# Kernel tuning notes

Measured on AMD Instinct MI355X. Metric: run time of the kernel, lower is better.

## Reference

```python
import jax, jax.numpy as jnp
import numpy as np

B, C, DM, H = 2, 256, 512, 8
D = DM // H          # d_head = 64
SPARSE_K = 64


def setup_inputs() -> dict:
    key = jax.random.key(0)
    ks = jax.random.split(key, 12)
    s = 0.02
    return {
        "x": jax.random.normal(ks[0], (B, C, DM), dtype=jnp.float32),
        "Wq": jax.random.normal(ks[1], (DM, DM), dtype=jnp.float32) * s,
        "bq": jnp.zeros((DM,), jnp.float32),
        "Wk": jax.random.normal(ks[2], (DM, DM), dtype=jnp.float32) * s,
        "bk": jnp.zeros((DM,), jnp.float32),
        "Wv": jax.random.normal(ks[3], (DM, DM), dtype=jnp.float32) * s,
        "bv": jnp.zeros((DM,), jnp.float32),
        "w1": jax.random.normal(ks[4], (D, 3 * D), dtype=jnp.float32) * s,
        "b1": jax.random.normal(ks[5], (D,), dtype=jnp.float32) * s,
        "w2": jax.random.normal(ks[6], (1, D), dtype=jnp.float32) * s,
        "b2": jax.random.normal(ks[7], (1,), dtype=jnp.float32) * s,
        "Wo": jax.random.normal(ks[8], (DM, DM), dtype=jnp.float32) * s,
        "bo": jnp.zeros((DM,), jnp.float32),
    }


def _heads(x, W, b):
    # torch Linear: x @ W.T + b, then (B,C,H,d) -> (B,H,C,d)
    y = jnp.einsum("bcD,ED->bcE", x, W) + b
    return y.reshape(B, C, H, D).transpose(0, 2, 1, 3)


def reference(x, Wq, bq, Wk, bk, Wv, bv, w1, b1, w2, b2, Wo, bo):
    q = _heads(x, Wq, bq)  # (B,H,C,d)
    k = _heads(x, Wk, bk)
    v = _heads(x, Wv, bv)

    # split first MLP layer weight: [:, :d] acts on q, [:, d:2d] on k, [:, 2d:] on q*k
    q_p = jnp.einsum("bhcd,ed->bhce", q, w1[:, :D])
    k_p = jnp.einsum("bhcd,ed->bhce", k, w1[:, D:2 * D])

    # res: (B,H,C,C,d)
    res = q_p[:, :, :, None, :] + k_p[:, :, None, :, :] + b1
    interaction = q[:, :, :, None, :] * k[:, :, None, :, :]
    res = res + jnp.einsum("bhije,fe->bhijf", interaction, w1[:, 2 * D:])

    # second MLP layer -> scalar score per pair, exact (erf) GELU as torch default
    h = jax.nn.gelu(res, approximate=False)
    scores = (jnp.einsum("bhijd,od->bhijo", h, w2) + b2)[..., 0]
    scores = scores / jnp.sqrt(jnp.float32(D))

    if SPARSE_K < C:
        top_vals = jax.lax.top_k(scores, SPARSE_K)[0]
        thresh = top_vals[..., -1:]
        scores = jnp.where(scores >= thresh, scores, jnp.float32(-1e9))

    attn = jax.nn.softmax(scores, axis=-1)  # dropout is identity (p=0 / eval)
    out = jnp.einsum("bhij,bhjd->bhid", attn, v)
    out = out.transpose(0, 2, 1, 3).reshape(B, C, DM)
    return jnp.einsum("bcD,ED->bcE", out, Wo) + bo
```

## Files before the change

### kernel.cpp

```cpp
#include <hip/hip_runtime.h>
#include <math.h>

typedef _Float16 fp16;
typedef __attribute__((ext_vector_type(4))) _Float16 f16x4;
typedef __attribute__((ext_vector_type(8))) _Float16 f16x8;
typedef __attribute__((ext_vector_type(4))) float floatx4;
typedef __attribute__((ext_vector_type(2))) float f32x2;

__device__ __forceinline__ f32x2 mk2(float a, float b) { f32x2 r; r.x = a; r.y = b; return r; }
__device__ __forceinline__ f32x2 sp2(float a) { f32x2 r; r.x = a; r.y = a; return r; }

__device__ __forceinline__ f32x2 gelu2(f32x2 x) {
    f32x2 tt = x * 0.70710678118654752440f;
    f32x2 s  = tt * tt;
    f32x2 p  = __builtin_elementwise_fma(s, sp2(-8.548327023450852e-4f), sp2(5.223977625442188e-3f));
    p = __builtin_elementwise_fma(s, p, sp2(-2.6866170645131252e-2f));
    p = __builtin_elementwise_fma(s, p, sp2(0.11283791670955126f));
    p = __builtin_elementwise_fma(s, p, sp2(-0.3761263890318375f));
    p = __builtin_elementwise_fma(s, p, sp2(1.1283791670955126f));
    f32x2 e = tt * p;
    if (__builtin_expect(fabsf(tt.x) > 0.5f, 0)) e.x = erff(tt.x);
    if (__builtin_expect(fabsf(tt.y) > 0.5f, 0)) e.y = erff(tt.y);
    f32x2 hx = x * 0.5f;
    return __builtin_elementwise_fma(hx, e, hx);
}

__device__ __forceinline__ void split2(float a, fp16& h, fp16& m) {
    h = (fp16)a;
    m = (fp16)(a - (float)h);
}

struct SplitArgs {
    const float* src[5];
    fp16* h[5]; fp16* m[5];
};

__global__ __launch_bounds__(256) void split2_512_kernel(SplitArgs S) {
    int z = blockIdx.z;
    const float* src = S.src[z];
    fp16* dh = S.h[z]; fp16* dm = S.m[z];
    int t = blockIdx.x * 256 + threadIdx.x;
    int row = t >> 7, kq = (t & 127) * 4;
    int rt = row >> 4, rm = row & 15;
    int ks = kq >> 5, q4 = (kq >> 3) & 3, u0 = kq & 7;
    int dst = ((rt * 16 + ks) * 64 + q4 * 16 + rm) * 8 + u0;
    float4 vv = *(const float4*)&src[row * 512 + kq];
    float a4[4] = {vv.x, vv.y, vv.z, vv.w};
    f16x4 h, m;
    #pragma unroll
    for (int u = 0; u < 4; u++) {
        fp16 hh, mm;
        split2(a4[u], hh, mm);
        h[u] = hh; m[u] = mm;
    }
    *(f16x4*)&dh[dst] = h;
    *(f16x4*)&dm[dst] = m;
}

struct MM2Args {
    const fp16 *Ah, *Am;
    const fp16 *Wh[3], *Wm[3];
    const float* bias[3];
    float* outf[3];
    fp16 *kh, *km;
    int mode[3];
};

__global__ __launch_bounds__(64) void mm_mfma_kernel(MM2Args A) {
    const int z = blockIdx.z;
    const fp16* Wh = A.Wh[z]; const fp16* Wm = A.Wm[z];
    const float* bias = A.bias[z];
    const int lane = threadIdx.x;
    const int m16 = lane & 15, q4 = lane >> 4;
    const int mt = blockIdx.y, bx = blockIdx.x;

    floatx4 acc0, acc1;
    {
        float bv = bias[bx * 16 + m16];
        acc0[0] = bv; acc0[1] = bv; acc0[2] = bv; acc0[3] = bv;
        acc1[0] = 0.f; acc1[1] = 0.f; acc1[2] = 0.f; acc1[3] = 0.f;
    }

    #pragma unroll 4
    for (int ks = 0; ks < 16; ks++) {
        int sa = ((mt * 16 + ks) * 64 + lane) * 8;
        f16x8 ah = *(const f16x8*)&A.Ah[sa];
        f16x8 am = *(const f16x8*)&A.Am[sa];
        int sw = ((bx * 16 + ks) * 64 + lane) * 8;
        f16x8 wh = *(const f16x8*)&Wh[sw];
        f16x8 wm = *(const f16x8*)&Wm[sw];
        acc0 = __builtin_amdgcn_mfma_f32_16x16x32_f16(ah, wh, acc0, 0, 0, 0);
        acc1 = __builtin_amdgcn_mfma_f32_16x16x32_f16(ah, wm, acc1, 0, 0, 0);
        acc0 = __builtin_amdgcn_mfma_f32_16x16x32_f16(am, wh, acc0, 0, 0, 0);
        acc1 = __builtin_amdgcn_mfma_f32_16x16x32_f16(am, wm, acc1, 0, 0, 0);
    }
    floatx4 acc = acc0 + acc1;

    const int mode = A.mode[z];
    const int n = bx * 16 + m16;
    #pragma unroll
    for (int r = 0; r < 4; r++) {
        int m = mt * 16 + q4 * 4 + r;
        float val = acc[r];
        if (mode == 0) {
            A.outf[z][m * 512 + n] = val;
        } else if (mode == 1) {
            A.outf[z][(((m >> 8) * 8 + (n >> 6)) * 256 + (m & 255)) * 64 + (n & 63)] = val;
        } else {
            int krow = ((m >> 8) * 8 + (n >> 6)) * 256 + (m & 255);
            int d = n & 63;
            int dst = (((krow >> 4) * 2 + (d >> 5)) * 64 + ((d >> 3) & 3) * 16 + (krow & 15)) * 8 + (d & 7);
            fp16 h, mm;
            split2(val, h, mm);
            A.kh[dst] = h; A.km[dst] = mm;
        }
    }
}

__global__ __launch_bounds__(256, 4) void fused_mfma_attn_kernel(
    const float* __restrict__ q, const float* __restrict__ v,
    const fp16* __restrict__ khi, const fp16* __restrict__ kmid,
    const float* __restrict__ w1, const float* __restrict__ b1,
    const float* __restrict__ w2, const float* __restrict__ b2,
    fp16* __restrict__ oh, fp16* __restrict__ om)
{
    const int i2 = blockIdx.x;
    const int bh = blockIdx.y;
    const int t  = threadIdx.x;
    const int lane = t & 63, w = t >> 6;
    const int m16 = lane & 15, q4 = lane >> 4;

    __shared__ f32x2 part2[4][256];
    __shared__ f32x2 sc2[256];
    __shared__ float qpb_s[2][64];
    __shared__ f32x2 sbuf2[256];
    __shared__ f32x2 red_s[4][64];
    __shared__ f32x2 red2_s[4];
    __shared__ f32x2 thr_s2, smax_s2;

    const int f = w * 16 + m16;
    const float* w1row = w1 + f * 192;

    f16x8 Ah[2][2], Am[2][2];
    #pragma unroll
    for (int i01 = 0; i01 < 2; i01++) {
        const float* qrow = q + (bh * 256 + i2 * 2 + i01) * 64;
        float qa = 0.f;
        #pragma unroll
        for (int ks = 0; ks < 2; ks++) {
            int e0 = ks * 32 + q4 * 8;
            #pragma unroll
            for (int u = 0; u < 2; u++) {
                int e = e0 + u * 4;
                float4 wa = *(const float4*)&w1row[e];
                float4 wb = *(const float4*)&w1row[64 + e];
                float4 wc = *(const float4*)&w1row[128 + e];
                float4 qv = *(const float4*)&qrow[e];
                qa += wa.x * qv.x + wa.y * qv.y + wa.z * qv.z + wa.w * qv.w;
                float av[4];
                av[0] = fmaf(wc.x, qv.x, wb.x);
                av[1] = fmaf(wc.y, qv.y, wb.y);
                av[2] = fmaf(wc.z, qv.z, wb.z);
                av[3] = fmaf(wc.w, qv.w, wb.w);
                #pragma unroll
                for (int uu = 0; uu < 4; uu++) {
                    fp16 h, m;
                    split2(av[uu], h, m);
                    Ah[i01][ks][u * 4 + uu] = h;
                    Am[i01][ks][u * 4 + uu] = m;
                }
            }
        }
        qa += __shfl_xor(qa, 16);
        qa += __shfl_xor(qa, 32);
        if (lane < 16) qpb_s[i01][w * 16 + lane] = qa + b1[w * 16 + lane];
    }
    __syncthreads();

    floatx4 qpbr[2];
    qpbr[0] = *(const floatx4*)&qpb_s[0][w * 16 + q4 * 4];
    qpbr[1] = *(const floatx4*)&qpb_s[1][w * 16 + q4 * 4];
    const float4 w2f = *(const float4*)&w2[w * 16 + q4 * 4];
    const float b2v = b2[0];

    {
        int base = ((bh * 16) * 2 * 64 + lane) * 8;
        f16x8 Kh0 = *(const f16x8*)&khi [base];
        f16x8 Km0 = *(const f16x8*)&kmid[base];
        f16x8 Kh1 = *(const f16x8*)&khi [base + 512];
        f16x8 Km1 = *(const f16x8*)&kmid[base + 512];
        #pragma unroll 1
        for (int jt = 0; jt < 16; jt++) {
            f16x8 nKh0, nKm0, nKh1, nKm1;
            if (jt < 15) {
                int nb = ((bh * 16 + jt + 1) * 2 * 64 + lane) * 8;
                nKh0 = *(const f16x8*)&khi [nb];
                nKm0 = *(const f16x8*)&kmid[nb];
                nKh1 = *(const f16x8*)&khi [nb + 512];
                nKm1 = *(const f16x8*)&kmid[nb + 512];
            }
            floatx4 a0 = qpbr[0], a1 = qpbr[1];
            floatx4 b0, b1v_;
            b0[0] = 0.f; b0[1] = 0.f; b0[2] = 0.f; b0[3] = 0.f;
            b1v_ = b0;
            a0   = __builtin_amdgcn_mfma_f32_16x16x32_f16(Ah[0][0], Kh0, a0,   0, 0, 0);
            a1   = __builtin_amdgcn_mfma_f32_16x16x32_f16(Ah[1][0], Kh0, a1,   0, 0, 0);
            b0   = __builtin_amdgcn_mfma_f32_16x16x32_f16(Ah[0][0], Km0, b0,   0, 0, 0);
            b1v_ = __builtin_amdgcn_mfma_f32_16x16x32_f16(Ah[1][0], Km0, b1v_, 0, 0, 0);
            a0   = __builtin_amdgcn_mfma_f32_16x16x32_f16(Am[0][0], Kh0, a0,   0, 0, 0);
            a1   = __builtin_amdgcn_mfma_f32_16x16x32_f16(Am[1][0], Kh0, a1,   0, 0, 0);
            b0   = __builtin_amdgcn_mfma_f32_16x16x32_f16(Am[0][0], Km0, b0,   0, 0, 0);
            b1v_ = __builtin_amdgcn_mfma_f32_16x16x32_f16(Am[1][0], Km0, b1v_, 0, 0, 0);
            a0   = __builtin_amdgcn_mfma_f32_16x16x32_f16(Ah[0][1], Kh1, a0,   0, 0, 0);
            a1   = __builtin_amdgcn_mfma_f32_16x16x32_f16(Ah[1][1], Kh1, a1,   0, 0, 0);
            b0   = __builtin_amdgcn_mfma_f32_16x16x32_f16(Ah[0][1], Km1, b0,   0, 0, 0);
            b1v_ = __builtin_amdgcn_mfma_f32_16x16x32_f16(Ah[1][1], Km1, b1v_, 0, 0, 0);
            a0   = __builtin_amdgcn_mfma_f32_16x16x32_f16(Am[0][1], Kh1, a0,   0, 0, 0);
            a1   = __builtin_amdgcn_mfma_f32_16x16x32_f16(Am[1][1], Kh1, a1,   0, 0, 0);
            b0   = __builtin_amdgcn_mfma_f32_16x16x32_f16(Am[0][1], Km1, b0,   0, 0, 0);
            b1v_ = __builtin_amdgcn_mfma_f32_16x16x32_f16(Am[1][1], Km1, b1v_, 0, 0, 0);
            a0 = a0 + b0; a1 = a1 + b1v_;
            f32x2 g0 = gelu2(mk2(a0[0], a1[0]));
            f32x2 g1 = gelu2(mk2(a0[1], a1[1]));
            f32x2 g2 = gelu2(mk2(a0[2], a1[2]));
            f32x2 g3 = gelu2(mk2(a0[3], a1[3]));
            f32x2 sA = __builtin_elementwise_fma(g1, sp2(w2f.y), g0 * w2f.x);
            f32x2 sB = __builtin_elementwise_fma(g3, sp2(w2f.w), g2 * w2f.z);
            f32x2 s = sA + sB;
            s.x += __shfl_xor(s.x, 16);
            s.y += __shfl_xor(s.y, 16);
            s.x += __shfl_xor(s.x, 32);
            s.y += __shfl_xor(s.y, 32);
            if (lane < 16) part2[w][jt * 16 + lane] = s;
            Kh0 = nKh0; Km0 = nKm0; Kh1 = nKh1; Km1 = nKm1;
        }
    }
    __syncthreads();

    f32x2 score = ((part2[0][t] + part2[1][t]) + (part2[2][t] + part2[3][t]) + b2v) * 0.125f;

    f32x2 sv = score;
    #pragma unroll
    for (int k = 2; k <= 256; k <<= 1) {
        #pragma unroll
        for (int j = k >> 1; j >= 1; j >>= 1) {
            f32x2 pv;
            if (j >= 64) {
                sbuf2[t] = sv;
                __syncthreads();
                pv = sbuf2[t ^ j];
                __syncthreads();
            } else {
                pv.x = __shfl_xor(sv.x, j);
                pv.y = __shfl_xor(sv.y, j);
            }
            bool keepMin = (((t & j) == 0) == ((t & k) == 0));
            f32x2 mn = __builtin_elementwise_min(sv, pv);
            f32x2 mx = __builtin_elementwise_max(sv, pv);
            sv = keepMin ? mn : mx;
        }
    }
    if (t == 192) thr_s2  = sv;
    if (t == 255) smax_s2 = sv;
    __syncthreads();

    float p0 = (score.x >= thr_s2.x) ? __expf(score.x - smax_s2.x) : 0.0f;
    float p1 = (score.y >= thr_s2.y) ? __expf(score.y - smax_s2.y) : 0.0f;
    sc2[t] = mk2(p0, p1);
    f32x2 ps = mk2(p0, p1);
    #pragma unroll
    for (int mask = 1; mask < 64; mask <<= 1) {
        ps.x += __shfl_xor(ps.x, mask);
        ps.y += __shfl_xor(ps.y, mask);
    }
    if (lane == 0) red2_s[w] = ps;
    __syncthreads();
    f32x2 den = (red2_s[0] + red2_s[1]) + (red2_s[2] + red2_s[3]);
    f32x2 invp = mk2(1.0f / den.x, 1.0f / den.y);

    const int d = t & 63, g = t >> 6;
    const float* vb = v + bh * 256 * 64;
    f32x2 av = mk2(0.f, 0.f), avb = mk2(0.f, 0.f);
    for (int j8 = 0; j8 < 8; j8++) {
        int jj = g * 64 + j8 * 8;
        f32x2 pp0 = sc2[jj + 0];
        f32x2 pp1 = sc2[jj + 1];
        f32x2 pp2 = sc2[jj + 2];
        f32x2 pp3 = sc2[jj + 3];
        f32x2 pp4 = sc2[jj + 4];
        f32x2 pp5 = sc2[jj + 5];
        f32x2 pp6 = sc2[jj + 6];
        f32x2 pp7 = sc2[jj + 7];
        float v0 = vb[(jj + 0) * 64 + d];
        float v1 = vb[(jj + 1) * 64 + d];
        float v2 = vb[(jj + 2) * 64 + d];
        float v3 = vb[(jj + 3) * 64 + d];
        float v4 = vb[(jj + 4) * 64 + d];
        float v5 = vb[(jj + 5) * 64 + d];
        float v6 = vb[(jj + 6) * 64 + d];
        float v7 = vb[(jj + 7) * 64 + d];
        av  = __builtin_elementwise_fma(pp0, sp2(v0), av);
        avb = __builtin_elementwise_fma(pp4, sp2(v4), avb);
        av  = __builtin_elementwise_fma(pp1, sp2(v1), av);
        avb = __builtin_elementwise_fma(pp5, sp2(v5), avb);
        av  = __builtin_elementwise_fma(pp2, sp2(v2), av);
        avb = __builtin_elementwise_fma(pp6, sp2(v6), avb);
        av  = __builtin_elementwise_fma(pp3, sp2(v3), av);
        avb = __builtin_elementwise_fma(pp7, sp2(v7), avb);
    }
    red_s[g][d] = av + avb;
    __syncthreads();

    if (t < 128) {
        int i01 = t >> 6, dd = t & 63;
        f32x2 osum = (red_s[0][dd] + red_s[1][dd]) + (red_s[2][dd] + red_s[3][dd]);
        float o = (i01 ? osum.y : osum.x) * (i01 ? invp.y : invp.x);
        int b = bh >> 3, h = bh & 7;
        int row = b * 256 + i2 * 2 + i01;
        int n = h * 64 + dd;
        int dst = (((row >> 4) * 16 + (n >> 5)) * 64 + ((n >> 3) & 3) * 16 + (row & 15)) * 8 + (n & 7);
        fp16 hh, mm;
        split2(o, hh, mm);
        oh[dst] = hh; om[dst] = mm;
    }
}

extern "C" void kernel_launch(void* const* d_in, const int* in_sizes, int n_in,
                              void* d_out, int out_size, void* d_ws, size_t ws_size,
                              hipStream_t stream) {
    const float* x  = (const float*)d_in[0];
    const float* Wq = (const float*)d_in[1];
    const float* bq = (const float*)d_in[2];
    const float* Wk = (const float*)d_in[3];
    const float* bk = (const float*)d_in[4];
    const float* Wv = (const float*)d_in[5];
    const float* bv = (const float*)d_in[6];
    const float* w1 = (const float*)d_in[7];
    const float* b1 = (const float*)d_in[8];
    const float* w2 = (const float*)d_in[9];
    const float* b2 = (const float*)d_in[10];
    const float* Wo = (const float*)d_in[11];
    const float* bo = (const float*)d_in[12];
    float* out = (float*)d_out;

    const int NE = 262144;
    float* qb  = (float*)d_ws;
    float* vb  = qb + NE;
    fp16* base = (fp16*)(vb + NE);
    fp16* khi  = base;            fp16* kmid = khi + NE;
    fp16* xs   = kmid + NE;
    fp16* wqs  = xs  + 2 * NE;
    fp16* wks  = wqs + 2 * NE;
    fp16* wvs  = wks + 2 * NE;
    fp16* wos  = wvs + 2 * NE;
    fp16* oas  = wos + 2 * NE;

    {
        SplitArgs S;
        const float* srcs[5] = {x, Wq, Wk, Wv, Wo};
        fp16* dsts[5] = {xs, wqs, wks, wvs, wos};
        for (int z = 0; z < 5; z++) {
            S.src[z] = srcs[z];
            S.h[z] = dsts[z]; S.m[z] = dsts[z] + NE;
        }
        split2_512_kernel<<<dim3(256, 1, 5), 256, 0, stream>>>(S);
    }
    {
        MM2Args M;
        M.Ah = xs; M.Am = xs + NE;
        M.Wh[0] = wqs; M.Wm[0] = wqs + NE;
        M.Wh[1] = wks; M.Wm[1] = wks + NE;
        M.Wh[2] = wvs; M.Wm[2] = wvs + NE;
        M.bias[0] = bq; M.bias[1] = bk; M.bias[2] = bv;
        M.outf[0] = qb; M.outf[1] = nullptr; M.outf[2] = vb;
        M.kh = khi; M.km = kmid;
        M.mode[0] = 1; M.mode[1] = 2; M.mode[2] = 1;
        mm_mfma_kernel<<<dim3(32, 32, 3), 64, 0, stream>>>(M);
    }
    fused_mfma_attn_kernel<<<dim3(128, 16), 256, 0, stream>>>(
        qb, vb, khi, kmid, w1, b1, w2, b2,
        oas, oas + NE);
    {
        MM2Args M;
        M.Ah = oas; M.Am = oas + NE;
        M.Wh[0] = wos; M.Wm[0] = wos + NE;
        M.Wh[1] = wos; M.Wm[1] = wos;
        M.Wh[2] = wos; M.Wm[2] = wos;
        M.bias[0] = bo; M.bias[1] = bo; M.bias[2] = bo;
        M.outf[0] = out; M.outf[1] = out; M.outf[2] = out;
        M.kh = khi; M.km = kmid;
        M.mode[0] = 0; M.mode[1] = 0; M.mode[2] = 0;
        mm_mfma_kernel<<<dim3(32, 32, 1), 64, 0, stream>>>(M);
    }
}
```

Baseline: 173.2 us.

## Process four query rows per attention block to reuse K fragments

```diff
diff --git a/kernel.cpp b/kernel.cpp
--- a/kernel.cpp
+++ b/kernel.cpp
@@ -117,46 +117,45 @@
     }
 }
 
-__global__ __launch_bounds__(256, 4) void fused_mfma_attn_kernel(
+__global__ __launch_bounds__(256, 3) void fused_mfma_attn_kernel(
     const float* __restrict__ q, const float* __restrict__ v,
     const fp16* __restrict__ khi, const fp16* __restrict__ kmid,
     const float* __restrict__ w1, const float* __restrict__ b1,
     const float* __restrict__ w2, const float* __restrict__ b2,
     fp16* __restrict__ oh, fp16* __restrict__ om)
 {
-    const int i2 = blockIdx.x;
+    const int i4 = blockIdx.x;
     const int bh = blockIdx.y;
     const int t  = threadIdx.x;
     const int lane = t & 63, w = t >> 6;
     const int m16 = lane & 15, q4 = lane >> 4;
 
-    __shared__ f32x2 part2[4][256];
-    __shared__ f32x2 sc2[256];
-    __shared__ float qpb_s[2][64];
-    __shared__ f32x2 sbuf2[256];
-    __shared__ f32x2 red_s[4][64];
-    __shared__ f32x2 red2_s[4];
-    __shared__ f32x2 thr_s2, smax_s2;
+    __shared__ f32x2 part2[2][4][256];
+    __shared__ f32x2 sc2[2][256];
+    __shared__ float qpb_s[4][64];
+    __shared__ f32x2 sbuf2[2][256];
+    __shared__ f32x2 red_s[2][4][64];
+    __shared__ f32x2 red2_s[2][4];
+    __shared__ f32x2 thr_s2[2], smax_s2[2];
 
     const int f = w * 16 + m16;
     const float* w1row = w1 + f * 192;
 
-    f16x8 Ah[2][2], Am[2][2];
-    #pragma unroll
-    for (int i01 = 0; i01 < 2; i01++) {
-        const float* qrow = q + (bh * 256 + i2 * 2 + i01) * 64;
-        float qa = 0.f;
+    f16x8 Ah[4][2], Am[4][2];
+    float qa[4] = {0.f, 0.f, 0.f, 0.f};
+    const float* qbase = q + (bh * 256 + i4 * 4) * 64;
+    #pragma unroll
+    for (int ks = 0; ks < 2; ks++) {
         #pragma unroll
-        for (int ks = 0; ks < 2; ks++) {
-            int e0 = ks * 32 + q4 * 8;
+        for (int u = 0; u < 2; u++) {
+            int e = ks * 32 + q4 * 8 + u * 4;
+            float4 wa = *(const float4*)&w1row[e];
+            float4 wb = *(const float4*)&w1row[64 + e];
+            float4 wc = *(const float4*)&w1row[128 + e];
             #pragma unroll
-            for (int u = 0; u < 2; u++) {
-                int e = e0 + u * 4;
-                float4 wa = *(const float4*)&w1row[e];
-                float4 wb = *(const float4*)&w1row[64 + e];
-                float4 wc = *(const float4*)&w1row[128 + e];
-                float4 qv = *(const float4*)&qrow[e];
-                qa += wa.x * qv.x + wa.y * qv.y + wa.z * qv.z + wa.w * qv.w;
+            for (int i01 = 0; i01 < 4; i01++) {
+                float4 qv = *(const float4*)&qbase[i01 * 64 + e];
+                qa[i01] += wa.x * qv.x + wa.y * qv.y + wa.z * qv.z + wa.w * qv.w;
                 float av[4];
                 av[0] = fmaf(wc.x, qv.x, wb.x);
                 av[1] = fmaf(wc.y, qv.y, wb.y);
@@ -171,15 +170,20 @@
                 }
             }
         }
-        qa += __shfl_xor(qa, 16);
-        qa += __shfl_xor(qa, 32);
-        if (lane < 16) qpb_s[i01][w * 16 + lane] = qa + b1[w * 16 + lane];
+    }
+    #pragma unroll
+    for (int i01 = 0; i01 < 4; i01++) {
+        float qaa = qa[i01];
+        qaa += __shfl_xor(qaa, 16);
+        qaa += __shfl_xor(qaa, 32);
+        if (lane < 16) qpb_s[i01][w * 16 + lane] = qaa + b1[w * 16 + lane];
     }
     __syncthreads();
 
-    floatx4 qpbr[2];
-    qpbr[0] = *(const floatx4*)&qpb_s[0][w * 16 + q4 * 4];
-    qpbr[1] = *(const floatx4*)&qpb_s[1][w * 16 + q4 * 4];
+    floatx4 qpbr[4];
+    #pragma unroll
+    for (int i01 = 0; i01 < 4; i01++)
+        qpbr[i01] = *(const floatx4*)&qpb_s[i01][w * 16 + q4 * 4];
     const float4 w2f = *(const float4*)&w2[w * 16 + q4 * 4];
     const float b2v = b2[0];
 
@@ -199,98 +203,110 @@
                 nKh1 = *(const f16x8*)&khi [nb + 512];
                 nKm1 = *(const f16x8*)&kmid[nb + 512];
             }
-            floatx4 a0 = qpbr[0], a1 = qpbr[1];
-            floatx4 b0, b1v_;
-            b0[0] = 0.f; b0[1] = 0.f; b0[2] = 0.f; b0[3] = 0.f;
-            b1v_ = b0;
-            a0   = __builtin_amdgcn_mfma_f32_16x16x32_f16(Ah[0][0], Kh0, a0,   0, 0, 0);
-            a1   = __builtin_amdgcn_mfma_f32_16x16x32_f16(Ah[1][0], Kh0, a1,   0, 0, 0);
-            b0   = __builtin_amdgcn_mfma_f32_16x16x32_f16(Ah[0][0], Km0, b0,   0, 0, 0);
-            b1v_ = __builtin_amdgcn_mfma_f32_16x16x32_f16(Ah[1][0], Km0, b1v_, 0, 0, 0);
-            a0   = __builtin_amdgcn_mfma_f32_16x16x32_f16(Am[0][0], Kh0, a0,   0, 0, 0);
-            a1   = __builtin_amdgcn_mfma_f32_16x16x32_f16(Am[1][0], Kh0, a1,   0, 0, 0);
-            b0   = __builtin_amdgcn_mfma_f32_16x16x32_f16(Am[0][0], Km0, b0,   0, 0, 0);
-            b1v_ = __builtin_amdgcn_mfma_f32_16x16x32_f16(Am[1][0], Km0, b1v_, 0, 0, 0);
-            a0   = __builtin_amdgcn_mfma_f32_16x16x32_f16(Ah[0][1], Kh1, a0,   0, 0, 0);
-            a1   = __builtin_amdgcn_mfma_f32_16x16x32_f16(Ah[1][1], Kh1, a1,   0, 0, 0);
-            b0   = __builtin_amdgcn_mfma_f32_16x16x32_f16(Ah[0][1], Km1, b0,   0, 0, 0);
-            b1v_ = __builtin_amdgcn_mfma_f32_16x16x32_f16(Ah[1][1], Km1, b1v_, 0, 0, 0);
-            a0   = __builtin_amdgcn_mfma_f32_16x16x32_f16(Am[0][1], Kh1, a0,   0, 0, 0);
-            a1   = __builtin_amdgcn_mfma_f32_16x16x32_f16(Am[1][1], Kh1, a1,   0, 0, 0);
-            b0   = __builtin_amdgcn_mfma_f32_16x16x32_f16(Am[0][1], Km1, b0,   0, 0, 0);
-            b1v_ = __builtin_amdgcn_mfma_f32_16x16x32_f16(Am[1][1], Km1, b1v_, 0, 0, 0);
-            a0 = a0 + b0; a1 = a1 + b1v_;
-            f32x2 g0 = gelu2(mk2(a0[0], a1[0]));
-            f32x2 g1 = gelu2(mk2(a0[1], a1[1]));
-            f32x2 g2 = gelu2(mk2(a0[2], a1[2]));
-            f32x2 g3 = gelu2(mk2(a0[3], a1[3]));
-            f32x2 sA = __builtin_elementwise_fma(g1, sp2(w2f.y), g0 * w2f.x);
-            f32x2 sB = __builtin_elementwise_fma(g3, sp2(w2f.w), g2 * w2f.z);
-            f32x2 s = sA + sB;
-            s.x += __shfl_xor(s.x, 16);
-            s.y += __shfl_xor(s.y, 16);
-            s.x += __shfl_xor(s.x, 32);
-            s.y += __shfl_xor(s.y, 32);
-            if (lane < 16) part2[w][jt * 16 + lane] = s;
+            #pragma unroll
+            for (int p = 0; p < 2; p++) {
+                const int ia = 2 * p, ib = 2 * p + 1;
+                floatx4 a0 = qpbr[ia], a1 = qpbr[ib];
+                floatx4 b0, b1v_;
+                b0[0] = 0.f; b0[1] = 0.f; b0[2] = 0.f; b0[3] = 0.f;
+                b1v_ = b0;
+                a0   = __builtin_amdgcn_mfma_f32_16x16x32_f16(Ah[ia][0], Kh0, a0,   0, 0, 0);
+                a1   = __builtin_amdgcn_mfma_f32_16x16x32_f16(Ah[ib][0], Kh0, a1,   0, 0, 0);
+                b0   = __builtin_amdgcn_mfma_f32_16x16x32_f16(Ah[ia][0], Km0, b0,   0, 0, 0);
+                b1v_ = __builtin_amdgcn_mfma_f32_16x16x32_f16(Ah[ib][0], Km0, b1v_, 0, 0, 0);
+                a0   = __builtin_amdgcn_mfma_f32_16x16x32_f16(Am[ia][0], Kh0, a0,   0, 0, 0);
+                a1   = __builtin_amdgcn_mfma_f32_16x16x32_f16(Am[ib][0], Kh0, a1,   0, 0, 0);
+                b0   = __builtin_amdgcn_mfma_f32_16x16x32_f16(Am[ia][0], Km0, b0,   0, 0, 0);
+                b1v_ = __builtin_amdgcn_mfma_f32_16x16x32_f16(Am[ib][0], Km0, b1v_, 0, 0, 0);
+                a0   = __builtin_amdgcn_mfma_f32_16x16x32_f16(Ah[ia][1], Kh1, a0,   0, 0, 0);
+                a1   = __builtin_amdgcn_mfma_f32_16x16x32_f16(Ah[ib][1], Kh1, a1,   0, 0, 0);
+                b0   = __builtin_amdgcn_mfma_f32_16x16x32_f16(Ah[ia][1], Km1, b0,   0, 0, 0);
+                b1v_ = __builtin_amdgcn_mfma_f32_16x16x32_f16(Ah[ib][1], Km1, b1v_, 0, 0, 0);
+                a0   = __builtin_amdgcn_mfma_f32_16x16x32_f16(Am[ia][1], Kh1, a0,   0, 0, 0);
+                a1   = __builtin_amdgcn_mfma_f32_16x16x32_f16(Am[ib][1], Kh1, a1,   0, 0, 0);
+                b0   = __builtin_amdgcn_mfma_f32_16x16x32_f16(Am[ia][1], Km1, b0,   0, 0, 0);
+                b1v_ = __builtin_amdgcn_mfma_f32_16x16x32_f16(Am[ib][1], Km1, b1v_, 0, 0, 0);
+                a0 = a0 + b0; a1 = a1 + b1v_;
+                f32x2 g0 = gelu2(mk2(a0[0], a1[0]));
+                f32x2 g1 = gelu2(mk2(a0[1], a1[1]));
+                f32x2 g2 = gelu2(mk2(a0[2], a1[2]));
+                f32x2 g3 = gelu2(mk2(a0[3], a1[3]));
+                f32x2 sA = __builtin_elementwise_fma(g1, sp2(w2f.y), g0 * w2f.x);
+                f32x2 sB = __builtin_elementwise_fma(g3, sp2(w2f.w), g2 * w2f.z);
+                f32x2 s = sA + sB;
+                s.x += __shfl_xor(s.x, 16);
+                s.y += __shfl_xor(s.y, 16);
+                s.x += __shfl_xor(s.x, 32);
+                s.y += __shfl_xor(s.y, 32);
+                if (lane < 16) part2[p][w][jt * 16 + lane] = s;
+            }
             Kh0 = nKh0; Km0 = nKm0; Kh1 = nKh1; Km1 = nKm1;
         }
     }
     __syncthreads();
 
-    f32x2 score = ((part2[0][t] + part2[1][t]) + (part2[2][t] + part2[3][t]) + b2v) * 0.125f;
-
-    f32x2 sv = score;
+    f32x2 score0 = ((part2[0][0][t] + part2[0][1][t]) +
+                    (part2[0][2][t] + part2[0][3][t]) + b2v) * 0.125f;
+    f32x2 score1 = ((part2[1][0][t] + part2[1][1][t]) +
+                    (part2[1][2][t] + part2[1][3][t]) + b2v) * 0.125f;
+
+    f32x2 sv0 = score0, sv1 = score1;
     #pragma unroll
     for (int k = 2; k <= 256; k <<= 1) {
         #pragma unroll
         for (int j = k >> 1; j >= 1; j >>= 1) {
-            f32x2 pv;
+            f32x2 pv0, pv1;
             if (j >= 64) {
-                sbuf2[t] = sv;
+                sbuf2[0][t] = sv0; sbuf2[1][t] = sv1;
                 __syncthreads();
-                pv = sbuf2[t ^ j];
+                pv0 = sbuf2[0][t ^ j]; pv1 = sbuf2[1][t ^ j];
                 __syncthreads();
             } else {
-                pv.x = __shfl_xor(sv.x, j);
-                pv.y = __shfl_xor(sv.y, j);
+                pv0.x = __shfl_xor(sv0.x, j);
+                pv0.y = __shfl_xor(sv0.y, j);
+                pv1.x = __shfl_xor(sv1.x, j);
+                pv1.y = __shfl_xor(sv1.y, j);
             }
             bool keepMin = (((t & j) == 0) == ((t & k) == 0));
-            f32x2 mn = __builtin_elementwise_min(sv, pv);
-            f32x2 mx = __builtin_elementwise_max(sv, pv);
-            sv = keepMin ? mn : mx;
+            f32x2 mn0 = __builtin_elementwise_min(sv0, pv0);
+            f32x2 mx0 = __builtin_elementwise_max(sv0, pv0);
+            f32x2 mn1 = __builtin_elementwise_min(sv1, pv1);
+            f32x2 mx1 = __builtin_elementwise_max(sv1, pv1);
+            sv0 = keepMin ? mn0 : mx0;
+            sv1 = keepMin ? mn1 : mx1;
         }
     }
-    if (t == 192) thr_s2  = sv;
-    if (t == 255) smax_s2 = sv;
+    if (t == 192) { thr_s2[0]  = sv0; thr_s2[1]  = sv1; }
+    if (t == 255) { smax_s2[0] = sv0; smax_s2[1] = sv1; }
     __syncthreads();
 
-    float p0 = (score.x >= thr_s2.x) ? __expf(score.x - smax_s2.x) : 0.0f;
-    float p1 = (score.y >= thr_s2.y) ? __expf(score.y - smax_s2.y) : 0.0f;
-    sc2[t] = mk2(p0, p1);
-    f32x2 ps = mk2(p0, p1);
+    float p00 = (score0.x >= thr_s2[0].x) ? __expf(score0.x - smax_s2[0].x) : 0.0f;
+    float p01 = (score0.y >= thr_s2[0].y) ? __expf(score0.y - smax_s2[0].y) : 0.0f;
+    float p10 = (score1.x >= thr_s2[1].x) ? __expf(score1.x - smax_s2[1].x) : 0.0f;
+    float p11 = (score1.y >= thr_s2[1].y) ? __expf(score1.y - smax_s2[1].y) : 0.0f;
+    sc2[0][t] = mk2(p00, p01);
+    sc2[1][t] = mk2(p10, p11);
+    f32x2 ps0 = mk2(p00, p01), ps1 = mk2(p10, p11);
     #pragma unroll
     for (int mask = 1; mask < 64; mask <<= 1) {
-        ps.x += __shfl_xor(ps.x, mask);
-        ps.y += __shfl_xor(ps.y, mask);
-    }
-    if (lane == 0) red2_s[w] = ps;
+        ps0.x += __shfl_xor(ps0.x, mask);
+        ps0.y += __shfl_xor(ps0.y, mask);
+        ps1.x += __shfl_xor(ps1.x, mask);
+        ps1.y += __shfl_xor(ps1.y, mask);
+    }
+    if (lane == 0) { red2_s[0][w] = ps0; red2_s[1][w] = ps1; }
     __syncthreads();
-    f32x2 den = (red2_s[0] + red2_s[1]) + (red2_s[2] + red2_s[3]);
-    f32x2 invp = mk2(1.0f / den.x, 1.0f / den.y);
+    f32x2 den0 = (red2_s[0][0] + red2_s[0][1]) + (red2_s[0][2] + red2_s[0][3]);
+    f32x2 den1 = (red2_s[1][0] + red2_s[1][1]) + (red2_s[1][2] + red2_s[1][3]);
+    f32x2 invp0 = mk2(1.0f / den0.x, 1.0f / den0.y);
+    f32x2 invp1 = mk2(1.0f / den1.x, 1.0f / den1.y);
 
     const int d = t & 63, g = t >> 6;
     const float* vb = v + bh * 256 * 64;
-    f32x2 av = mk2(0.f, 0.f), avb = mk2(0.f, 0.f);
+    f32x2 av0 = mk2(0.f, 0.f), av1 = mk2(0.f, 0.f);
+    f32x2 av0b = mk2(0.f, 0.f), av1b = mk2(0.f, 0.f);
     for (int j8 = 0; j8 < 8; j8++) {
         int jj = g * 64 + j8 * 8;
-        f32x2 pp0 = sc2[jj + 0];
-        f32x2 pp1 = sc2[jj + 1];
-        f32x2 pp2 = sc2[jj + 2];
-        f32x2 pp3 = sc2[jj + 3];
-        f32x2 pp4 = sc2[jj + 4];
-        f32x2 pp5 = sc2[jj + 5];
-        f32x2 pp6 = sc2[jj + 6];
-        f32x2 pp7 = sc2[jj + 7];
         float v0 = vb[(jj + 0) * 64 + d];
         float v1 = vb[(jj + 1) * 64 + d];
         float v2 = vb[(jj + 2) * 64 + d];
@@ -299,24 +315,36 @@
         float v5 = vb[(jj + 5) * 64 + d];
         float v6 = vb[(jj + 6) * 64 + d];
         float v7 = vb[(jj + 7) * 64 + d];
-        av  = __builtin_elementwise_fma(pp0, sp2(v0), av);
-        avb = __builtin_elementwise_fma(pp4, sp2(v4), avb);
-        av  = __builtin_elementwise_fma(pp1, sp2(v1), av);
-        avb = __builtin_elementwise_fma(pp5, sp2(v5), avb);
-        av  = __builtin_elementwise_fma(pp2, sp2(v2), av);
-        avb = __builtin_elementwise_fma(pp6, sp2(v6), avb);
-        av  = __builtin_elementwise_fma(pp3, sp2(v3), av);
-        avb = __builtin_elementwise_fma(pp7, sp2(v7), avb);
-    }
-    red_s[g][d] = av + avb;
+        av0  = __builtin_elementwise_fma(sc2[0][jj + 0], sp2(v0), av0);
+        av1  = __builtin_elementwise_fma(sc2[1][jj + 0], sp2(v0), av1);
+        av0b = __builtin_elementwise_fma(sc2[0][jj + 4], sp2(v4), av0b);
+        av1b = __builtin_elementwise_fma(sc2[1][jj + 4], sp2(v4), av1b);
+        av0  = __builtin_elementwise_fma(sc2[0][jj + 1], sp2(v1), av0);
+        av1  = __builtin_elementwise_fma(sc2[1][jj + 1], sp2(v1), av1);
+        av0b = __builtin_elementwise_fma(sc2[0][jj + 5], sp2(v5), av0b);
+        av1b = __builtin_elementwise_fma(sc2[1][jj + 5], sp2(v5), av1b);
+        av0  = __builtin_elementwise_fma(sc2[0][jj + 2], sp2(v2), av0);
+        av1  = __builtin_elementwise_fma(sc2[1][jj + 2], sp2(v2), av1);
+        av0b = __builtin_elementwise_fma(sc2[0][jj + 6], sp2(v6), av0b);
+        av1b = __builtin_elementwise_fma(sc2[1][jj + 6], sp2(v6), av1b);
+        av0  = __builtin_elementwise_fma(sc2[0][jj + 3], sp2(v3), av0);
+        av1  = __builtin_elementwise_fma(sc2[1][jj + 3], sp2(v3), av1);
+        av0b = __builtin_elementwise_fma(sc2[0][jj + 7], sp2(v7), av0b);
+        av1b = __builtin_elementwise_fma(sc2[1][jj + 7], sp2(v7), av1b);
+    }
+    red_s[0][g][d] = av0 + av0b;
+    red_s[1][g][d] = av1 + av1b;
     __syncthreads();
 
-    if (t < 128) {
+    {
         int i01 = t >> 6, dd = t & 63;
-        f32x2 osum = (red_s[0][dd] + red_s[1][dd]) + (red_s[2][dd] + red_s[3][dd]);
-        float o = (i01 ? osum.y : osum.x) * (i01 ? invp.y : invp.x);
+        int pr = i01 >> 1, comp = i01 & 1;
+        f32x2 osum = (red_s[pr][0][dd] + red_s[pr][1][dd]) +
+                     (red_s[pr][2][dd] + red_s[pr][3][dd]);
+        f32x2 iv = pr ? invp1 : invp0;
+        float o = (comp ? osum.y : osum.x) * (comp ? iv.y : iv.x);
         int b = bh >> 3, h = bh & 7;
-        int row = b * 256 + i2 * 2 + i01;
+        int row = b * 256 + i4 * 4 + i01;
         int n = h * 64 + dd;
         int dst = (((row >> 4) * 16 + (n >> 5)) * 64 + ((n >> 3) & 3) * 16 + (row & 15)) * 8 + (n & 7);
         fp16 hh, mm;
@@ -377,7 +405,7 @@
         M.mode[0] = 1; M.mode[1] = 2; M.mode[2] = 1;
         mm_mfma_kernel<<<dim3(32, 32, 3), 64, 0, stream>>>(M);
     }
-    fused_mfma_attn_kernel<<<dim3(128, 16), 256, 0, stream>>>(
+    fused_mfma_attn_kernel<<<dim3(64, 16), 256, 0, stream>>>(
         qb, vb, khi, kmid, w1, b1, w2, b2,
         oas, oas + NE);
     {
```

After: 170.1 us. No clear change (-1.8%).
